# Optimization experiments

Measured on AMD Instinct MI355X. Metric: run time of the kernel, lower is better.

Reference implementation:

```python
import jax, jax.numpy as jnp
import numpy as np
import math

B, S, H, NH = 2, 2048, 2048, 16
HD = H // NH            # head_dim = 128
SEQ_LENGTH = 1024       # config.seq_length (logn base)
NEG = -1e9


def _rotate_half(x):
    # x: [..., hd]; split into two halves (j=2 layout) and rotate
    d = x.shape[-1] // 2
    x1, x2 = x[..., :d], x[..., d:]
    return jnp.concatenate([-x2, x1], axis=-1)


def _apply_rope(t, cos, sin):
    # t: [B,S,NH,HD], cos/sin: [1,S,1,rot_dim]; rot_dim == HD here (no pass-through)
    return t * cos + _rotate_half(t) * sin


def setup_inputs() -> dict:
    key = jax.random.key(0)
    k0, k1, k2 = jax.random.split(key, 3)
    hidden_states = jax.random.normal(k0, (B, S, H), jnp.float32)

    # rotary cos/sin: QWen-style, freqs duplicated across both halves
    pos = jnp.arange(S, dtype=jnp.float32)
    inv_freq = 1.0 / (10000.0 ** (jnp.arange(0, HD, 2, dtype=jnp.float32) / HD))  # [HD/2]
    ang = pos[:, None] * inv_freq[None, :]                # [S, HD/2]
    ang = jnp.concatenate([ang, ang], axis=-1)[None, :, None, :]  # [1,S,1,HD]
    cos, sin = jnp.cos(ang), jnp.sin(ang)

    # additive causal mask (registered_causal_mask path is unused in _attn)
    causal = jnp.tril(jnp.ones((S, S), dtype=bool))
    attention_mask = jnp.where(causal, 0.0, NEG)[None, None, :, :].astype(jnp.float32)

    # logn scaling vector for positions 1..S
    i = np.arange(1, S + 1)
    logn_np = np.where(i > SEQ_LENGTH, np.log(i) / np.log(SEQ_LENGTH), 1.0).astype(np.float32)
    logn = jnp.asarray(logn_np)[None, :, None, None]      # [1,S,1,1]

    Wc = jax.random.normal(k1, (H, 3 * H), jnp.float32) * 0.02
    bc = jnp.zeros((3 * H,), jnp.float32)
    Wp = jax.random.normal(k2, (H, H), jnp.float32) * 0.02
    bp = jnp.zeros((H,), jnp.float32)
    return {
        "hidden_states": hidden_states, "cos": cos, "sin": sin,
        "attention_mask": attention_mask, "logn": logn,
        "Wc": Wc, "bc": bc, "Wp": Wp, "bp": bp,
    }


def reference(hidden_states, cos, sin, attention_mask, logn, Wc, bc, Wp, bp):
    # QKV projection
    qkv = hidden_states @ Wc + bc                         # [B,S,3H]
    q, k, v = jnp.split(qkv, 3, axis=-1)
    q = q.reshape(B, S, NH, HD)
    k = k.reshape(B, S, NH, HD)
    v = v.reshape(B, S, NH, HD)

    # rotary embedding on q and k
    q = _apply_rope(q, cos, sin)
    k = _apply_rope(k, cos, sin)

    # logn attention scaling (eval mode): q *= log_{seq_length}(pos) for pos>seq_length
    q = q * logn

    # [B,NH,S,HD]
    q = q.transpose(0, 2, 1, 3)
    k = k.transpose(0, 2, 1, 3)
    v = v.transpose(0, 2, 1, 3)

    scale = 1.0 / math.sqrt(HD)
    scores = jnp.einsum("bhqd,bhkd->bhqk", q, k) * scale + attention_mask
    attn = jax.nn.softmax(scores, axis=-1)
    ctx = jnp.einsum("bhqk,bhkd->bhqd", attn, v)          # [B,NH,S,HD]
    ctx = ctx.transpose(0, 2, 1, 3).reshape(B, S, H)      # merge heads
    return ctx @ Wp + bp                                  # [B,S,H]
```

## Files before the change

kernel.cpp:

```cpp
#include <hip/hip_runtime.h>

#define Bsz 2
#define Ssz 2048
#define Hsz 2048
#define NHsz 16
#define HDsz 128
#define K3sz 6144
#define Msz 4096

typedef _Float16 f16x8 __attribute__((ext_vector_type(8)));
typedef float f32x4 __attribute__((ext_vector_type(4)));

typedef __attribute__((address_space(3))) void lds_void;
typedef __attribute__((address_space(1))) void glob_void;
__device__ __forceinline__ void async_copy16(void* lds, const void* g) {
  __builtin_amdgcn_global_load_lds((const glob_void*)g, (lds_void*)lds, 16, 0, 0);
}

__global__ __launch_bounds__(256)
void cvt_f32_f16(const float* __restrict__ in, _Float16* __restrict__ out) {
  size_t i = ((size_t)blockIdx.x * 256 + threadIdx.x) * 8;
  float4 a = *(const float4*)(in + i);
  float4 b = *(const float4*)(in + i + 4);
  f16x8 v;
  v[0] = (_Float16)a.x; v[1] = (_Float16)a.y; v[2] = (_Float16)a.z; v[3] = (_Float16)a.w;
  v[4] = (_Float16)b.x; v[5] = (_Float16)b.y; v[6] = (_Float16)b.z; v[7] = (_Float16)b.w;
  *(f16x8*)(out + i) = v;
}

__global__ __launch_bounds__(256)
void wtrans(const float* __restrict__ W, _Float16* __restrict__ WT, int N, int K) {
  __shared__ _Float16 T[64][72];
  const int t = threadIdx.x;
  const int n0 = blockIdx.x * 64, k0 = blockIdx.y * 64;
#pragma unroll
  for (int i = 0; i < 4; ++i) {
    int c = i * 256 + t;
    int rr = c >> 4, c4 = c & 15;
    float4 v = *(const float4*)(W + (size_t)(k0 + rr) * N + n0 + c4 * 4);
    T[c4 * 4 + 0][rr] = (_Float16)v.x;
    T[c4 * 4 + 1][rr] = (_Float16)v.y;
    T[c4 * 4 + 2][rr] = (_Float16)v.z;
    T[c4 * 4 + 3][rr] = (_Float16)v.w;
  }
  __syncthreads();
#pragma unroll
  for (int i = 0; i < 2; ++i) {
    int c = i * 256 + t;
    int nn = c >> 3, k8 = c & 7;
    *(f16x8*)(WT + (size_t)(n0 + nn) * K + k0 + k8 * 8) = *(const f16x8*)&T[nn][k8 * 8];
  }
}

template<typename CT>
__global__ __launch_bounds__(256)
void gemm_f16(const _Float16* __restrict__ A, int lda,
              const _Float16* __restrict__ BT,
              const float* __restrict__ bias,
              CT* __restrict__ C, int ldc, int K) {
  __shared__ _Float16 As[128][64];
  __shared__ _Float16 Bs[128][64];
  const int t = threadIdx.x;
  const int w = t >> 6, l = t & 63, lg = l >> 4, ll = l & 15;
  const int wr = w >> 1, wc = w & 1;
  const int m0 = blockIdx.y * 128, c0 = blockIdx.x * 128;

  const int srow = l >> 3;
  const int swz = ((l & 7) ^ (srow & 7)) * 8;
  const size_t aRow = (size_t)(m0 + w * 32 + srow);
  const size_t bRow = (size_t)(c0 + w * 32 + srow);

  f32x4 acc[4][4];
#pragma unroll
  for (int mf = 0; mf < 4; ++mf)
#pragma unroll
    for (int nf = 0; nf < 4; ++nf)
#pragma unroll
      for (int r = 0; r < 4; ++r) acc[mf][nf][r] = 0.f;

  for (int k0 = 0; k0 < K; k0 += 64) {
#pragma unroll
    for (int i = 0; i < 4; ++i) {
      int ldsOff = (w * 32 + i * 8) * 128 + l * 16;
      async_copy16((char*)As + ldsOff, A  + (aRow + i * 8) * lda + k0 + swz);
      async_copy16((char*)Bs + ldsOff, BT + (bRow + i * 8) * K   + k0 + swz);
    }
    __syncthreads();
#pragma unroll
    for (int ks = 0; ks < 2; ++ks) {
      f16x8 af[4], bf[4];
#pragma unroll
      for (int x = 0; x < 4; ++x) {
        int cA = ((ks * 4 + lg) ^ (ll & 7)) * 8;
        af[x] = *(const f16x8*)&As[wr * 64 + x * 16 + ll][cA];
        bf[x] = *(const f16x8*)&Bs[wc * 64 + x * 16 + ll][cA];
      }
#pragma unroll
      for (int mf = 0; mf < 4; ++mf)
#pragma unroll
        for (int nf = 0; nf < 4; ++nf)
          acc[mf][nf] = __builtin_amdgcn_mfma_f32_16x16x32_f16(af[mf], bf[nf], acc[mf][nf], 0, 0, 0);
    }
    __syncthreads();
  }
#pragma unroll
  for (int mf = 0; mf < 4; ++mf)
#pragma unroll
    for (int nf = 0; nf < 4; ++nf) {
      int col = c0 + wc * 64 + nf * 16 + ll;
      float bv = bias[col];
#pragma unroll
      for (int r = 0; r < 4; ++r) {
        int row = m0 + wr * 64 + mf * 16 + lg * 4 + r;
        C[(size_t)row * ldc + col] = (CT)(acc[mf][nf][r] + bv);
      }
    }
}

__global__ __launch_bounds__(256)
void rope_cvt(_Float16* __restrict__ qkv, const float* __restrict__ cosb,
              const float* __restrict__ sinb, const float* __restrict__ logn,
              _Float16* __restrict__ Kh) {
  int idx = blockIdx.x * 256 + threadIdx.x;
  int d = idx & 63;
  int h = (idx >> 6) & 15;
  int s = (idx >> 10) & 2047;
  int b = idx >> 21;
  size_t base = ((size_t)(b * Ssz + s)) * K3sz + h * HDsz;
  float c1 = cosb[s * HDsz + d];
  float s1 = sinb[s * HDsz + d];
  float c2 = cosb[s * HDsz + 64 + d];
  float s2 = sinb[s * HDsz + 64 + d];
  float ln = logn[s] * 0.08838834764831845f;
  float q1 = (float)qkv[base + d], q2 = (float)qkv[base + 64 + d];
  float k1 = (float)qkv[base + Hsz + d], k2 = (float)qkv[base + Hsz + 64 + d];
  qkv[base + d]      = (_Float16)((q1 * c1 - q2 * s1) * ln);
  qkv[base + 64 + d] = (_Float16)((q2 * c2 + q1 * s2) * ln);
  size_t ko = ((size_t)((b * NHsz + h) * Ssz + s)) * HDsz;
  Kh[ko + d]      = (_Float16)(k1 * c1 - k2 * s1);
  Kh[ko + 64 + d] = (_Float16)(k2 * c2 + k1 * s2);
}

__global__ __launch_bounds__(256)
void vtrans(const _Float16* __restrict__ qkv, _Float16* __restrict__ Vt) {
  __shared__ _Float16 T[128][72];
  const int t = threadIdx.x;
  const int s0 = blockIdx.x * 64;
  const int h = blockIdx.y;
  const int b = blockIdx.z;
#pragma unroll
  for (int i = 0; i < 4; ++i) {
    int c = i * 256 + t;
    int rr = c >> 4, c8 = c & 15;
    f16x8 v = *(const f16x8*)(qkv + ((size_t)(b * Ssz + s0 + rr)) * K3sz + 2 * Hsz + h * HDsz + c8 * 8);
#pragma unroll
    for (int j = 0; j < 8; ++j) T[c8 * 8 + j][rr] = v[j];
  }
  __syncthreads();
  _Float16* Vg = Vt + (size_t)(b * NHsz + h) * (Ssz * HDsz);
#pragma unroll
  for (int i = 0; i < 4; ++i) {
    int c = i * 256 + t;
    int d = c >> 3, s8 = c & 7;
    *(f16x8*)(Vg + (size_t)d * Ssz + s0 + s8 * 8) = *(const f16x8*)&T[d][s8 * 8];
  }
}

__global__ __launch_bounds__(256)
void flash_mfma(_Float16* __restrict__ qkv, const _Float16* __restrict__ Kh,
                const _Float16* __restrict__ Vt) {
  __shared__ _Float16 Ks[64][128];
  __shared__ _Float16 Vs[128][64];
  __shared__ _Float16 Ps[4][16][64];
  const int t = threadIdx.x;
  const int w = t >> 6, l = t & 63, lg = l >> 4, ll = l & 15;
  const int qblk = 31 - (int)blockIdx.x;
  const int h = blockIdx.y, b = blockIdx.z;
  const size_t bh = (size_t)(b * NHsz + h);

  const int qrow_g = qblk * 64 + w * 16 + ll;
  f16x8 qf[4];
  {
    const _Float16* qrow = qkv + ((size_t)(b * Ssz) + qrow_g) * K3sz + h * HDsz;
#pragma unroll
    for (int kds = 0; kds < 4; ++kds)
      qf[kds] = *(const f16x8*)(qrow + kds * 32 + lg * 8);
  }

  f32x4 O[8];
#pragma unroll
  for (int nf = 0; nf < 8; ++nf)
#pragma unroll
    for (int r = 0; r < 4; ++r) O[nf][r] = 0.f;
  float m[4] = {-1e30f, -1e30f, -1e30f, -1e30f};
  float lp[4] = {0.f, 0.f, 0.f, 0.f};

  const _Float16* Kg = Kh + bh * (size_t)(Ssz * HDsz);
  const _Float16* Vg = Vt + bh * (size_t)(Ssz * HDsz);

  int kSrc[4], kLds[4], vSrc[4], vLds[4];
#pragma unroll
  for (int i = 0; i < 4; ++i) {
    int krow = w * 16 + i * 4 + (l >> 4);
    kSrc[i] = krow * 128 + (((l & 15) ^ (krow & 7)) * 8);
    kLds[i] = (w * 16 + i * 4) * 256 + l * 16;
    int vrow = w * 32 + i * 8 + (l >> 3);
    vSrc[i] = vrow * Ssz + (((l & 7) ^ (vrow & 7)) * 8);
    vLds[i] = (w * 32 + i * 8) * 128 + l * 16;
  }

  for (int kt = 0; kt <= qblk; ++kt) {
    const _Float16* Ktile = Kg + (size_t)kt * (64 * HDsz);
    const _Float16* Vtile = Vg + kt * 64;
#pragma unroll
    for (int i = 0; i < 4; ++i) {
      async_copy16((char*)Ks + kLds[i], Ktile + kSrc[i]);
      async_copy16((char*)Vs + vLds[i], Vtile + vSrc[i]);
    }
    __syncthreads();

    f32x4 S[4];
#pragma unroll
    for (int kf = 0; kf < 4; ++kf) {
#pragma unroll
      for (int r = 0; r < 4; ++r) S[kf][r] = 0.f;
#pragma unroll
      for (int kds = 0; kds < 4; ++kds) {
        f16x8 bk = *(const f16x8*)&Ks[kf * 16 + ll][(((kds * 4 + lg) ^ (ll & 7))) * 8];
        S[kf] = __builtin_amdgcn_mfma_f32_16x16x32_f16(qf[kds], bk, S[kf], 0, 0, 0);
      }
    }
    if (kt == qblk) {
#pragma unroll
      for (int kf = 0; kf < 4; ++kf) {
        int kcol = kt * 64 + kf * 16 + ll;
#pragma unroll
        for (int r = 0; r < 4; ++r) {
          int qg = qblk * 64 + w * 16 + lg * 4 + r;
          if (kcol > qg) S[kf][r] = -1e30f;
        }
      }
    }

    float pmax[4];
    bool need = false;
#pragma unroll
    for (int r = 0; r < 4; ++r) {
      float v = fmaxf(fmaxf(S[0][r], S[1][r]), fmaxf(S[2][r], S[3][r]));
      v = fmaxf(v, __shfl_xor(v, 1));
      v = fmaxf(v, __shfl_xor(v, 2));
      v = fmaxf(v, __shfl_xor(v, 4));
      v = fmaxf(v, __shfl_xor(v, 8));
      pmax[r] = v;
      need = need || (v > m[r] + 8.f);
    }
    if (__any(need)) {
#pragma unroll
      for (int r = 0; r < 4; ++r) {
        float mn = fmaxf(m[r], pmax[r]);
        float corr = __expf(m[r] - mn);
        lp[r] *= corr;
#pragma unroll
        for (int nf = 0; nf < 8; ++nf) O[nf][r] *= corr;
        m[r] = mn;
      }
    }
#pragma unroll
    for (int r = 0; r < 4; ++r) {
      int q7 = (lg * 4 + r) & 7;
      float p0 = __expf(S[0][r] - m[r]);
      float p1 = __expf(S[1][r] - m[r]);
      float p2 = __expf(S[2][r] - m[r]);
      float p3 = __expf(S[3][r] - m[r]);
      lp[r] += (p0 + p1) + (p2 + p3);
      int u = ll >> 3, s = ll & 7;
      Ps[w][lg * 4 + r][((0 + u) ^ q7) * 8 + s] = (_Float16)p0;
      Ps[w][lg * 4 + r][((2 + u) ^ q7) * 8 + s] = (_Float16)p1;
      Ps[w][lg * 4 + r][((4 + u) ^ q7) * 8 + s] = (_Float16)p2;
      Ps[w][lg * 4 + r][((6 + u) ^ q7) * 8 + s] = (_Float16)p3;
    }
    f16x8 pa0 = *(const f16x8*)&Ps[w][ll][((lg ^ (ll & 7))) * 8];
    f16x8 pa1 = *(const f16x8*)&Ps[w][ll][(((4 + lg) ^ (ll & 7))) * 8];
#pragma unroll
    for (int nf = 0; nf < 8; ++nf) {
      f16x8 vb0 = *(const f16x8*)&Vs[nf * 16 + ll][((lg ^ (ll & 7))) * 8];
      f16x8 vb1 = *(const f16x8*)&Vs[nf * 16 + ll][(((4 + lg) ^ (ll & 7))) * 8];
      O[nf] = __builtin_amdgcn_mfma_f32_16x16x32_f16(pa0, vb0, O[nf], 0, 0, 0);
      O[nf] = __builtin_amdgcn_mfma_f32_16x16x32_f16(pa1, vb1, O[nf], 0, 0, 0);
    }
    __syncthreads();
  }

#pragma unroll
  for (int r = 0; r < 4; ++r) {
    float s = lp[r];
    s += __shfl_xor(s, 1);
    s += __shfl_xor(s, 2);
    s += __shfl_xor(s, 4);
    s += __shfl_xor(s, 8);
    float inv = 1.f / s;
    _Float16* crow = qkv + ((size_t)(b * Ssz) + qblk * 64 + w * 16 + lg * 4 + r) * K3sz + h * HDsz;
#pragma unroll
    for (int nf = 0; nf < 8; ++nf)
      crow[nf * 16 + ll] = (_Float16)(O[nf][r] * inv);
  }
}

extern "C" void kernel_launch(void* const* d_in, const int* in_sizes, int n_in,
                              void* d_out, int out_size, void* d_ws, size_t ws_size,
                              hipStream_t stream) {
  const float* hs   = (const float*)d_in[0];
  const float* cosb = (const float*)d_in[1];
  const float* sinb = (const float*)d_in[2];
  const float* logn = (const float*)d_in[4];
  const float* Wc   = (const float*)d_in[5];
  const float* bc   = (const float*)d_in[6];
  const float* Wp   = (const float*)d_in[7];
  const float* bp   = (const float*)d_in[8];
  float* out = (float*)d_out;

  _Float16* qkv  = (_Float16*)d_ws;
  _Float16* hsF  = qkv  + (size_t)Msz * K3sz;
  _Float16* WcT  = hsF  + (size_t)Msz * Hsz;
  _Float16* WpT  = WcT  + (size_t)K3sz * Hsz;
  _Float16* Kh   = WpT  + (size_t)Hsz * Hsz;
  _Float16* Vt   = Kh   + (size_t)Bsz * NHsz * Ssz * HDsz;

  cvt_f32_f16<<<(Msz * Hsz) / (256 * 8), 256, 0, stream>>>(hs, hsF);
  { dim3 g(K3sz / 64, Hsz / 64); wtrans<<<g, 256, 0, stream>>>(Wc, WcT, K3sz, Hsz); }
  { dim3 g(Hsz / 64, Hsz / 64);  wtrans<<<g, 256, 0, stream>>>(Wp, WpT, Hsz, Hsz); }

  {
    dim3 g(K3sz / 128, Msz / 128);
    gemm_f16<_Float16><<<g, 256, 0, stream>>>(hsF, Hsz, WcT, bc, qkv, K3sz, Hsz);
  }
  rope_cvt<<<(Bsz * Ssz * NHsz * 64) / 256, 256, 0, stream>>>(qkv, cosb, sinb, logn, Kh);
  {
    dim3 g(Ssz / 64, NHsz, Bsz);
    vtrans<<<g, 256, 0, stream>>>(qkv, Vt);
  }
  {
    dim3 g(Ssz / 64, NHsz, Bsz);
    flash_mfma<<<g, 256, 0, stream>>>(qkv, Kh, Vt);
  }
  {
    dim3 g(Hsz / 128, Msz / 128);
    gemm_f16<float><<<g, 256, 0, stream>>>(qkv, K3sz, WpT, bp, out, Hsz, Hsz);
  }
}
```

Before: 495.8 us.

## Double-buffer K/V tiles and process 128 query rows per flash block

The flash attention kernel now double-buffers K and V tiles in LDS, issuing async loads for the next tile before computing on the current one and waiting with explicit vmcnt counts. Each block covers 128 query rows, with each wave handling two 16-row groups, so every K/V fragment read from LDS feeds twice as many MFMAs. The grid is reordered to put heads on x and to reverse query-block order for the second batch, to balance the causal workload. LDS use and register pressure roughly double, which may reduce occupancy.

```diff
diff --git a/kernel.cpp b/kernel.cpp
--- a/kernel.cpp
+++ b/kernel.cpp
@@ -169,31 +169,37 @@
 __global__ __launch_bounds__(256)
 void flash_mfma(_Float16* __restrict__ qkv, const _Float16* __restrict__ Kh,
                 const _Float16* __restrict__ Vt) {
-  __shared__ _Float16 Ks[64][128];
-  __shared__ _Float16 Vs[128][64];
-  __shared__ _Float16 Ps[4][16][64];
+  __shared__ _Float16 Ks[2][64][128];
+  __shared__ _Float16 Vs[2][128][64];
+  __shared__ _Float16 Ps[4][2][16][64];
   const int t = threadIdx.x;
   const int w = t >> 6, l = t & 63, lg = l >> 4, ll = l & 15;
-  const int qblk = 31 - (int)blockIdx.x;
-  const int h = blockIdx.y, b = blockIdx.z;
+  const int h = blockIdx.x;
+  const int qblk = (blockIdx.z == 0) ? (int)blockIdx.y : (15 - (int)blockIdx.y);
+  const int b = blockIdx.z;
   const size_t bh = (size_t)(b * NHsz + h);
 
-  const int qrow_g = qblk * 64 + w * 16 + ll;
-  f16x8 qf[4];
-  {
-    const _Float16* qrow = qkv + ((size_t)(b * Ssz) + qrow_g) * K3sz + h * HDsz;
+  f16x8 qf[2][4];
+#pragma unroll
+  for (int mg = 0; mg < 2; ++mg) {
+    const _Float16* qrow = qkv + ((size_t)(b * Ssz) + qblk * 128 + w * 32 + mg * 16 + ll) * K3sz + h * HDsz;
 #pragma unroll
     for (int kds = 0; kds < 4; ++kds)
-      qf[kds] = *(const f16x8*)(qrow + kds * 32 + lg * 8);
-  }
-
-  f32x4 O[8];
-#pragma unroll
-  for (int nf = 0; nf < 8; ++nf)
-#pragma unroll
-    for (int r = 0; r < 4; ++r) O[nf][r] = 0.f;
-  float m[4] = {-1e30f, -1e30f, -1e30f, -1e30f};
-  float lp[4] = {0.f, 0.f, 0.f, 0.f};
+      qf[mg][kds] = *(const f16x8*)(qrow + kds * 32 + lg * 8);
+  }
+
+  f32x4 O[2][8];
+#pragma unroll
+  for (int mg = 0; mg < 2; ++mg)
+#pragma unroll
+    for (int nf = 0; nf < 8; ++nf)
+#pragma unroll
+      for (int r = 0; r < 4; ++r) O[mg][nf][r] = 0.f;
+  float m[2][4], lp[2][4];
+#pragma unroll
+  for (int mg = 0; mg < 2; ++mg)
+#pragma unroll
+    for (int r = 0; r < 4; ++r) { m[mg][r] = -1e30f; lp[mg][r] = 0.f; }
 
   const _Float16* Kg = Kh + bh * (size_t)(Ssz * HDsz);
   const _Float16* Vg = Vt + bh * (size_t)(Ssz * HDsz);
@@ -209,101 +215,138 @@
     vLds[i] = (w * 32 + i * 8) * 128 + l * 16;
   }
 
-  for (int kt = 0; kt <= qblk; ++kt) {
-    const _Float16* Ktile = Kg + (size_t)kt * (64 * HDsz);
-    const _Float16* Vtile = Vg + kt * 64;
-#pragma unroll
-    for (int i = 0; i < 4; ++i) {
-      async_copy16((char*)Ks + kLds[i], Ktile + kSrc[i]);
-      async_copy16((char*)Vs + vLds[i], Vtile + vSrc[i]);
-    }
-    __syncthreads();
-
-    f32x4 S[4];
-#pragma unroll
-    for (int kf = 0; kf < 4; ++kf) {
-#pragma unroll
-      for (int r = 0; r < 4; ++r) S[kf][r] = 0.f;
+  const int nt = 2 * qblk + 2;
+#pragma unroll
+  for (int i = 0; i < 4; ++i) {
+    async_copy16((char*)Ks[0] + kLds[i], Kg + kSrc[i]);
+    async_copy16((char*)Vs[0] + vLds[i], Vg + vSrc[i]);
+  }
+  int cb = 0;
+
+  for (int kt = 0; kt < nt; ++kt) {
+    if (kt + 1 < nt) {
+      const _Float16* Ktile = Kg + (size_t)(kt + 1) * (64 * HDsz);
+      const _Float16* Vtile = Vg + (kt + 1) * 64;
+#pragma unroll
+      for (int i = 0; i < 4; ++i) {
+        async_copy16((char*)Ks[cb ^ 1] + kLds[i], Ktile + kSrc[i]);
+        async_copy16((char*)Vs[cb ^ 1] + vLds[i], Vtile + vSrc[i]);
+      }
+      asm volatile("s_waitcnt vmcnt(8)" ::: "memory");
+    } else {
+      asm volatile("s_waitcnt vmcnt(0)" ::: "memory");
+    }
+    __builtin_amdgcn_sched_barrier(0);
+    __builtin_amdgcn_s_barrier();
+    __builtin_amdgcn_sched_barrier(0);
+
+    f32x4 S[2][4];
+#pragma unroll
+    for (int mg = 0; mg < 2; ++mg)
+#pragma unroll
+      for (int kf = 0; kf < 4; ++kf)
+#pragma unroll
+        for (int r = 0; r < 4; ++r) S[mg][kf][r] = 0.f;
+#pragma unroll
+    for (int kf = 0; kf < 4; ++kf)
 #pragma unroll
       for (int kds = 0; kds < 4; ++kds) {
-        f16x8 bk = *(const f16x8*)&Ks[kf * 16 + ll][(((kds * 4 + lg) ^ (ll & 7))) * 8];
-        S[kf] = __builtin_amdgcn_mfma_f32_16x16x32_f16(qf[kds], bk, S[kf], 0, 0, 0);
-      }
-    }
-    if (kt == qblk) {
-#pragma unroll
-      for (int kf = 0; kf < 4; ++kf) {
-        int kcol = kt * 64 + kf * 16 + ll;
+        f16x8 bk = *(const f16x8*)&Ks[cb][kf * 16 + ll][(((kds * 4 + lg) ^ (ll & 7))) * 8];
+        S[0][kf] = __builtin_amdgcn_mfma_f32_16x16x32_f16(qf[0][kds], bk, S[0][kf], 0, 0, 0);
+        S[1][kf] = __builtin_amdgcn_mfma_f32_16x16x32_f16(qf[1][kds], bk, S[1][kf], 0, 0, 0);
+      }
+    if (kt >= 2 * qblk) {
+#pragma unroll
+      for (int mg = 0; mg < 2; ++mg)
+#pragma unroll
+        for (int kf = 0; kf < 4; ++kf) {
+          int kcol = kt * 64 + kf * 16 + ll;
+#pragma unroll
+          for (int r = 0; r < 4; ++r) {
+            int qg = qblk * 128 + w * 32 + mg * 16 + lg * 4 + r;
+            if (kcol > qg) S[mg][kf][r] = -1e30f;
+          }
+        }
+    }
+
+    float pmax[2][4];
+    bool need = false;
+#pragma unroll
+    for (int mg = 0; mg < 2; ++mg)
+#pragma unroll
+      for (int r = 0; r < 4; ++r) {
+        float v = fmaxf(fmaxf(S[mg][0][r], S[mg][1][r]), fmaxf(S[mg][2][r], S[mg][3][r]));
+        v = fmaxf(v, __shfl_xor(v, 1));
+        v = fmaxf(v, __shfl_xor(v, 2));
+        v = fmaxf(v, __shfl_xor(v, 4));
+        v = fmaxf(v, __shfl_xor(v, 8));
+        pmax[mg][r] = v;
+        need = need || (v > m[mg][r] + 8.f);
+      }
+    if (__any(need)) {
+#pragma unroll
+      for (int mg = 0; mg < 2; ++mg)
 #pragma unroll
         for (int r = 0; r < 4; ++r) {
-          int qg = qblk * 64 + w * 16 + lg * 4 + r;
-          if (kcol > qg) S[kf][r] = -1e30f;
+          float mn = fmaxf(m[mg][r], pmax[mg][r]);
+          float corr = __expf(m[mg][r] - mn);
+          lp[mg][r] *= corr;
+#pragma unroll
+          for (int nf = 0; nf < 8; ++nf) O[mg][nf][r] *= corr;
+          m[mg][r] = mn;
         }
-      }
-    }
-
-    float pmax[4];
-    bool need = false;
+    }
+#pragma unroll
+    for (int mg = 0; mg < 2; ++mg)
+#pragma unroll
+      for (int r = 0; r < 4; ++r) {
+        int q7 = (lg * 4 + r) & 7;
+        float p0 = __expf(S[mg][0][r] - m[mg][r]);
+        float p1 = __expf(S[mg][1][r] - m[mg][r]);
+        float p2 = __expf(S[mg][2][r] - m[mg][r]);
+        float p3 = __expf(S[mg][3][r] - m[mg][r]);
+        lp[mg][r] += (p0 + p1) + (p2 + p3);
+        int u = ll >> 3, s = ll & 7;
+        Ps[w][mg][lg * 4 + r][((0 + u) ^ q7) * 8 + s] = (_Float16)p0;
+        Ps[w][mg][lg * 4 + r][((2 + u) ^ q7) * 8 + s] = (_Float16)p1;
+        Ps[w][mg][lg * 4 + r][((4 + u) ^ q7) * 8 + s] = (_Float16)p2;
+        Ps[w][mg][lg * 4 + r][((6 + u) ^ q7) * 8 + s] = (_Float16)p3;
+      }
+    f16x8 pa[2][2];
+#pragma unroll
+    for (int mg = 0; mg < 2; ++mg) {
+      pa[mg][0] = *(const f16x8*)&Ps[w][mg][ll][((lg ^ (ll & 7))) * 8];
+      pa[mg][1] = *(const f16x8*)&Ps[w][mg][ll][(((4 + lg) ^ (ll & 7))) * 8];
+    }
+#pragma unroll
+    for (int nf = 0; nf < 8; ++nf) {
+      f16x8 vb0 = *(const f16x8*)&Vs[cb][nf * 16 + ll][((lg ^ (ll & 7))) * 8];
+      f16x8 vb1 = *(const f16x8*)&Vs[cb][nf * 16 + ll][(((4 + lg) ^ (ll & 7))) * 8];
+      O[0][nf] = __builtin_amdgcn_mfma_f32_16x16x32_f16(pa[0][0], vb0, O[0][nf], 0, 0, 0);
+      O[0][nf] = __builtin_amdgcn_mfma_f32_16x16x32_f16(pa[0][1], vb1, O[0][nf], 0, 0, 0);
+      O[1][nf] = __builtin_amdgcn_mfma_f32_16x16x32_f16(pa[1][0], vb0, O[1][nf], 0, 0, 0);
+      O[1][nf] = __builtin_amdgcn_mfma_f32_16x16x32_f16(pa[1][1], vb1, O[1][nf], 0, 0, 0);
+    }
+    __builtin_amdgcn_sched_barrier(0);
+    __builtin_amdgcn_s_barrier();
+    cb ^= 1;
+  }
+
+#pragma unroll
+  for (int mg = 0; mg < 2; ++mg)
 #pragma unroll
     for (int r = 0; r < 4; ++r) {
-      float v = fmaxf(fmaxf(S[0][r], S[1][r]), fmaxf(S[2][r], S[3][r]));
-      v = fmaxf(v, __shfl_xor(v, 1));
-      v = fmaxf(v, __shfl_xor(v, 2));
-      v = fmaxf(v, __shfl_xor(v, 4));
-      v = fmaxf(v, __shfl_xor(v, 8));
-      pmax[r] = v;
-      need = need || (v > m[r] + 8.f);
-    }
-    if (__any(need)) {
-#pragma unroll
-      for (int r = 0; r < 4; ++r) {
-        float mn = fmaxf(m[r], pmax[r]);
-        float corr = __expf(m[r] - mn);
-        lp[r] *= corr;
-#pragma unroll
-        for (int nf = 0; nf < 8; ++nf) O[nf][r] *= corr;
-        m[r] = mn;
-      }
-    }
-#pragma unroll
-    for (int r = 0; r < 4; ++r) {
-      int q7 = (lg * 4 + r) & 7;
-      float p0 = __expf(S[0][r] - m[r]);
-      float p1 = __expf(S[1][r] - m[r]);
-      float p2 = __expf(S[2][r] - m[r]);
-      float p3 = __expf(S[3][r] - m[r]);
-      lp[r] += (p0 + p1) + (p2 + p3);
-      int u = ll >> 3, s = ll & 7;
-      Ps[w][lg * 4 + r][((0 + u) ^ q7) * 8 + s] = (_Float16)p0;
-      Ps[w][lg * 4 + r][((2 + u) ^ q7) * 8 + s] = (_Float16)p1;
-      Ps[w][lg * 4 + r][((4 + u) ^ q7) * 8 + s] = (_Float16)p2;
-      Ps[w][lg * 4 + r][((6 + u) ^ q7) * 8 + s] = (_Float16)p3;
-    }
-    f16x8 pa0 = *(const f16x8*)&Ps[w][ll][((lg ^ (ll & 7))) * 8];
-    f16x8 pa1 = *(const f16x8*)&Ps[w][ll][(((4 + lg) ^ (ll & 7))) * 8];
-#pragma unroll
-    for (int nf = 0; nf < 8; ++nf) {
-      f16x8 vb0 = *(const f16x8*)&Vs[nf * 16 + ll][((lg ^ (ll & 7))) * 8];
-      f16x8 vb1 = *(const f16x8*)&Vs[nf * 16 + ll][(((4 + lg) ^ (ll & 7))) * 8];
-      O[nf] = __builtin_amdgcn_mfma_f32_16x16x32_f16(pa0, vb0, O[nf], 0, 0, 0);
-      O[nf] = __builtin_amdgcn_mfma_f32_16x16x32_f16(pa1, vb1, O[nf], 0, 0, 0);
-    }
-    __syncthreads();
-  }
-
-#pragma unroll
-  for (int r = 0; r < 4; ++r) {
-    float s = lp[r];
-    s += __shfl_xor(s, 1);
-    s += __shfl_xor(s, 2);
-    s += __shfl_xor(s, 4);
-    s += __shfl_xor(s, 8);
-    float inv = 1.f / s;
-    _Float16* crow = qkv + ((size_t)(b * Ssz) + qblk * 64 + w * 16 + lg * 4 + r) * K3sz + h * HDsz;
-#pragma unroll
-    for (int nf = 0; nf < 8; ++nf)
-      crow[nf * 16 + ll] = (_Float16)(O[nf][r] * inv);
-  }
+      float s = lp[mg][r];
+      s += __shfl_xor(s, 1);
+      s += __shfl_xor(s, 2);
+      s += __shfl_xor(s, 4);
+      s += __shfl_xor(s, 8);
+      float inv = 1.f / s;
+      _Float16* crow = qkv + ((size_t)(b * Ssz) + qblk * 128 + w * 32 + mg * 16 + lg * 4 + r) * K3sz + h * HDsz;
+#pragma unroll
+      for (int nf = 0; nf < 8; ++nf)
+        crow[nf * 16 + ll] = (_Float16)(O[mg][nf][r] * inv);
+    }
 }
 
 extern "C" void kernel_launch(void* const* d_in, const int* in_sizes, int n_in,
@@ -340,7 +383,7 @@
     vtrans<<<g, 256, 0, stream>>>(qkv, Vt);
   }
   {
-    dim3 g(Ssz / 64, NHsz, Bsz);
+    dim3 g(NHsz, Ssz / 128, Bsz);
     flash_mfma<<<g, 256, 0, stream>>>(qkv, Kh, Vt);
   }
   {
```

After: 448.3 us. 1.11x faster.
